# Kernel optimization log

Hardware: AMD Instinct MI355X
Metric: run time of the kernel (lower is better)

## Reference

```python
import jax, jax.numpy as jnp
import numpy as np

OUT, N_GROUPS, GROUP = 11008, 32, 128
IN = N_GROUPS * GROUP  # 4096
RANK = 128
B, S = 1, 64


def setup_inputs() -> dict:
    key = jax.random.key(0)
    ks = jax.random.split(key, 7)
    x = jax.random.normal(ks[0], (B, S, IN), dtype=jnp.float32)
    weight = jax.random.randint(ks[1], (OUT, N_GROUPS, GROUP), 0, 16, dtype=jnp.int32)
    scale = jax.random.uniform(ks[2], (OUT, N_GROUPS), dtype=jnp.float32) * 0.02 + 1e-3
    zero_point = jax.random.uniform(ks[3], (OUT, N_GROUPS), dtype=jnp.float32) * 15.0
    svd_up = jax.random.normal(ks[4], (OUT, RANK), dtype=jnp.float32) * 0.02
    svd_down = jax.random.normal(ks[5], (RANK, IN), dtype=jnp.float32) * 0.02
    bias = jax.random.normal(ks[6], (OUT,), dtype=jnp.float32) * 0.01
    return {"x": x, "weight": weight, "scale": scale, "zero_point": zero_point,
            "svd_up": svd_up, "svd_down": svd_down, "bias": bias}


def _dequantize(weight, scale, zero_point, svd_up, svd_down):
    # group-wise dequant: (W_q - zp) * scale, per (out, group) pair
    W = (weight.astype(jnp.float32) - zero_point[:, :, None]) * scale[:, :, None]
    W = W.reshape(weight.shape[0], -1)  # [OUT, IN]
    # low-rank SVD correction
    return W + svd_up @ svd_down


def reference(x, weight, scale, zero_point, svd_up, svd_down, bias):
    # int8 dynamic-quant path (token count 64 >= 16, int8_matmul=True)
    xt = x.reshape(-1, x.shape[-1])                       # [T, IN]
    W_f = _dequantize(weight, scale, zero_point, svd_up, svd_down).T  # [IN, OUT]
    scale_x = jnp.max(jnp.abs(xt), axis=1, keepdims=True) / 127.0     # [T, 1]
    x_q = jnp.clip(jnp.round(xt / scale_x), -128, 127).astype(jnp.int8)
    scale_w = jnp.max(jnp.abs(W_f), axis=0, keepdims=True) / 127.0    # [1, OUT]
    W_q8 = jnp.clip(jnp.round(W_f / scale_w), -128, 127).astype(jnp.int8)
    acc = jnp.matmul(x_q, W_q8, preferred_element_type=jnp.int32)     # [T, OUT] int32
    out = acc.astype(jnp.float32) * scale_x * scale_w
    return out[None] + bias  # [1, T, OUT], matching torch's unsqueeze(0) + bias
```

## Files before the change

### kernel.cpp

```cpp
#include <hip/hip_runtime.h>
#include <string.h>

#define OUT_DIM 11008
#define IN_DIM  4096
#define NTOK    64
#define RANK    128
#define NG      32
#define KSPLIT  8

typedef float        v4f  __attribute__((ext_vector_type(4)));
typedef int          v4i  __attribute__((ext_vector_type(4)));
typedef unsigned int v4u  __attribute__((ext_vector_type(4)));
typedef unsigned int v2u  __attribute__((ext_vector_type(2)));
typedef _Float16     v8h  __attribute__((ext_vector_type(8)));

__device__ inline unsigned int pack2h(float lo, float hi) {
  union { _Float16 h[2]; unsigned int u; } t;
  t.h[0] = (_Float16)lo; t.h[1] = (_Float16)hi;
  return t.u;
}

__global__ __launch_bounds__(256) void pack_d_kernel(const float* __restrict__ d,
                                                     unsigned int* __restrict__ dp) {
  int idx = (blockIdx.x * 256 + threadIdx.x) * 4;
  int r2 = idx >> 12, c = idx & 4095;
  v4f a = *(const v4f*)(d + (2 * r2) * IN_DIM + c);
  v4f b = *(const v4f*)(d + (2 * r2 + 1) * IN_DIM + c);
  v4u o;
#pragma unroll
  for (int e = 0; e < 4; e++) o[e] = pack2h(a[e], b[e]);
  *(v4u*)(dp + idx) = o;
}

__device__ inline void load_u(const float* __restrict__ svd_up, _Float16 (*U)[136],
                              int tid, int r0) {
#pragma unroll
  for (int i = 0; i < 16; i++) {
    int idx = i * 256 + tid;
    int r = idx >> 7, k = idx & 127;
    U[r][k] = (_Float16)svd_up[(r0 + r) * RANK + k];
  }
}

__device__ inline void stage_d(const unsigned int* __restrict__ dp, unsigned int (*Dl)[128],
                               int tid, int kt) {
  int c = (tid & 31) * 4;
#pragma unroll
  for (int i = 0; i < 8; i++) {
    int r2 = i * 8 + (tid >> 5);
    *(v4u*)&Dl[r2][c] = *(const v4u*)(dp + r2 * IN_DIM + kt * 128 + c);
  }
}

__device__ inline void svd_mfma(const _Float16 (*U)[136], const unsigned int (*Dl)[128],
                                int l, int w, v4f acc[2][2]) {
#pragma unroll
  for (int ks = 0; ks < 4; ks++) {
    v8h a0 = *(const v8h*)&U[(l & 15)][ks * 32 + (l >> 4) * 8];
    v8h a1 = *(const v8h*)&U[16 + (l & 15)][ks * 32 + (l >> 4) * 8];
#pragma unroll
    for (int fn = 0; fn < 2; fn++) {
      int col = w * 32 + fn * 16 + (l & 15);
      int rb = ks * 16 + (l >> 4) * 4;
      union { unsigned int u[4]; v8h h; } bu;
      bu.u[0] = Dl[rb][col];
      bu.u[1] = Dl[rb + 1][col];
      bu.u[2] = Dl[rb + 2][col];
      bu.u[3] = Dl[rb + 3][col];
      acc[0][fn] = __builtin_amdgcn_mfma_f32_16x16x32_f16(a0, bu.h, acc[0][fn], 0, 0, 0);
      acc[1][fn] = __builtin_amdgcn_mfma_f32_16x16x32_f16(a1, bu.h, acc[1][fn], 0, 0, 0);
    }
  }
}

__global__ __launch_bounds__(256) void cgemm_kernel(const float* __restrict__ svd_up,
    const unsigned int* __restrict__ dp, _Float16* __restrict__ Cb) {
  __shared__ _Float16 U[32][136];
  __shared__ unsigned int Dl[64][128];
  __shared__ _Float16 Clh[32][136];
  int tid = threadIdx.x;
  int r0 = blockIdx.x * 32;
  load_u(svd_up, U, tid, r0);
  int l = tid & 63, w = tid >> 6;
  int srow = tid >> 3, sc = (tid & 7) * 16;
  __syncthreads();
  for (int ct = 0; ct < 4; ct++) {
    int ktile = blockIdx.y * 4 + ct;
    stage_d(dp, Dl, tid, ktile);
    __syncthreads();
    v4f acc[2][2] = {};
    svd_mfma(U, Dl, l, w, acc);
#pragma unroll
    for (int fm = 0; fm < 2; fm++)
#pragma unroll
      for (int fn = 0; fn < 2; fn++)
#pragma unroll
        for (int j = 0; j < 4; j++)
          Clh[fm * 16 + (l >> 4) * 4 + j][w * 32 + fn * 16 + (l & 15)] = (_Float16)acc[fm][fn][j];
    __syncthreads();
    _Float16* dst = Cb + (r0 + srow) * IN_DIM + ktile * 128 + sc;
    *(v4u*)dst       = *(const v4u*)&Clh[srow][sc];
    *(v4u*)(dst + 8) = *(const v4u*)&Clh[srow][sc + 8];
  }
}

__global__ __launch_bounds__(256) void rowmax_kernel(const int* __restrict__ wq,
    const float* __restrict__ scale, const float* __restrict__ zp,
    const _Float16* __restrict__ Cb, unsigned int* __restrict__ wpk,
    float* __restrict__ swmax) {
  int tid = threadIdx.x;
  int lane = tid & 63, w = tid >> 6;
  int r = blockIdx.x * 4 + w;
  const int* wrow = wq + r * IN_DIM;
  const _Float16* crow = Cb + r * IN_DIM;
  unsigned int* prow = wpk + r * (IN_DIM / 8);
  const float* srow = scale + r * NG;
  const float* zrow = zp + r * NG;
  float m = 0.f;
#pragma unroll 4
  for (int j = 0; j < 8; j++) {
    int d = j * 64 + lane;
    int e0 = d * 8;
    v4i w0 = *(const v4i*)(wrow + e0);
    v4i w1 = *(const v4i*)(wrow + e0 + 4);
    union { v4u u; _Float16 h[8]; } cc;
    cc.u = *(const v4u*)(crow + e0);
    int g = e0 >> 7;
    float s = srow[g], z = zrow[g];
    unsigned int o = (unsigned)(w0[0] & 15)         | ((unsigned)(w0[1] & 15) << 4)
                   | ((unsigned)(w0[2] & 15) << 8)  | ((unsigned)(w0[3] & 15) << 12)
                   | ((unsigned)(w1[0] & 15) << 16) | ((unsigned)(w1[1] & 15) << 20)
                   | ((unsigned)(w1[2] & 15) << 24) | ((unsigned)(w1[3] & 15) << 28);
    prow[d] = o;
#pragma unroll
    for (int k = 0; k < 4; k++) {
      m = fmaxf(m, fabsf(((float)w0[k] - z) * s + (float)cc.h[k]));
      m = fmaxf(m, fabsf(((float)w1[k] - z) * s + (float)cc.h[k + 4]));
    }
  }
#pragma unroll
  for (int off = 1; off < 64; off <<= 1) m = fmaxf(m, __shfl_xor(m, off));
  if (lane == 0) swmax[r] = m;
}

__global__ __launch_bounds__(256) void quant_x_kernel(const float* __restrict__ x,
                                                      signed char* __restrict__ xq,
                                                      float* __restrict__ sx) {
  int t = blockIdx.x, tid = threadIdx.x;
  const float* row = x + t * IN_DIM;
  v4f v[4];
  float m = 0.f;
#pragma unroll
  for (int i = 0; i < 4; i++) {
    v[i] = *(const v4f*)(row + tid * 16 + i * 4);
#pragma unroll
    for (int e = 0; e < 4; e++) m = fmaxf(m, fabsf(v[i][e]));
  }
#pragma unroll
  for (int off = 1; off < 64; off <<= 1) m = fmaxf(m, __shfl_xor(m, off));
  __shared__ float wm[4];
  if ((tid & 63) == 0) wm[tid >> 6] = m;
  __syncthreads();
  m = fmaxf(fmaxf(wm[0], wm[1]), fmaxf(wm[2], wm[3]));
  float s = m / 127.0f;
  if (tid == 0) sx[t] = s;
  unsigned int packed[4];
#pragma unroll
  for (int i = 0; i < 4; i++) {
    int q[4];
#pragma unroll
    for (int e = 0; e < 4; e++) {
      float qf = rintf(v[i][e] / s);
      qf = fminf(127.f, fmaxf(-128.f, qf));
      q[e] = (int)qf;
    }
    packed[i] = (q[0] & 255) | ((q[1] & 255) << 8) | ((q[2] & 255) << 16) | ((q[3] & 255) << 24);
  }
  *(v4u*)(xq + t * IN_DIM + tid * 16) = *(v4u*)packed;
}

__global__ __launch_bounds__(256) void matmul_kernel(const unsigned int* __restrict__ wpk,
    const float* __restrict__ scale, const float* __restrict__ zp,
    const _Float16* __restrict__ Cb, const signed char* __restrict__ xq,
    const float* __restrict__ swmax, int* __restrict__ pacc) {
  __shared__ unsigned int W8[32][33];
  int tid = threadIdx.x;
  int r0 = blockIdx.x * 32;
  int kc = blockIdx.y;
  int l = tid & 63, w = tid >> 6;
  int myrow = tid >> 3, c0 = (tid & 7) * 16;
  float swr = swmax[r0 + myrow] / 127.0f;
  v4i oacc[2] = {};
  for (int kt = 0; kt < 4; kt++) {
    int kbase = kc * 512 + kt * 128;
    int g = kbase >> 7;
    float s = scale[(r0 + myrow) * NG + g];
    float z = zp[(r0 + myrow) * NG + g];
    v2u pk = *(const v2u*)(wpk + (r0 + myrow) * (IN_DIM / 8) + ((kbase + c0) >> 3));
    union { v4u u[2]; _Float16 h[16]; } cc;
    cc.u[0] = *(const v4u*)(Cb + (r0 + myrow) * IN_DIM + kbase + c0);
    cc.u[1] = *(const v4u*)(Cb + (r0 + myrow) * IN_DIM + kbase + c0 + 8);
    unsigned int wd[4];
#pragma unroll
    for (int i = 0; i < 4; i++) {
      int q[4];
#pragma unroll
      for (int e = 0; e < 4; e++) {
        int jj = i * 4 + e;
        int qn = (pk[jj >> 3] >> (4 * (jj & 7))) & 15;
        float W = ((float)qn - z) * s + (float)cc.h[jj];
        float qf = rintf(W / swr);
        qf = fminf(127.f, fmaxf(-128.f, qf));
        q[e] = (int)qf;
      }
      wd[i] = (q[0] & 255) | ((q[1] & 255) << 8) | ((q[2] & 255) << 16) | ((q[3] & 255) << 24);
    }
    __syncthreads();
#pragma unroll
    for (int i = 0; i < 4; i++) W8[myrow][(c0 >> 2) + i] = wd[i];
    __syncthreads();
#pragma unroll
    for (int ks = 0; ks < 2; ks++) {
      v4i a = *(const v4i*)(xq + (w * 16 + (l & 15)) * IN_DIM + kbase + ks * 64 + (l >> 4) * 16);
#pragma unroll
      for (int fr = 0; fr < 2; fr++) {
        int rr = fr * 16 + (l & 15);
        int kd = ks * 16 + (l >> 4) * 4;
        v4i b;
        b[0] = (int)W8[rr][kd];
        b[1] = (int)W8[rr][kd + 1];
        b[2] = (int)W8[rr][kd + 2];
        b[3] = (int)W8[rr][kd + 3];
        oacc[fr] = __builtin_amdgcn_mfma_i32_16x16x64_i8(a, b, oacc[fr], 0, 0, 0);
      }
    }
  }
  int* slab = pacc + kc * (NTOK * OUT_DIM);
#pragma unroll
  for (int fr = 0; fr < 2; fr++)
#pragma unroll
    for (int j = 0; j < 4; j++) {
      int token = w * 16 + (l >> 4) * 4 + j;
      int orow = r0 + fr * 16 + (l & 15);
      slab[token * OUT_DIM + orow] = oacc[fr][j];
    }
}

__global__ __launch_bounds__(256) void epilogue_kernel(const int* __restrict__ pacc,
    const float* __restrict__ sx, const float* __restrict__ swmax,
    const float* __restrict__ bias, float* __restrict__ out) {
  int o = blockIdx.x * 256 + threadIdx.x;
  int t = blockIdx.y;
  int acc = 0;
#pragma unroll
  for (int kc = 0; kc < KSPLIT; kc++)
    acc += pacc[kc * (NTOK * OUT_DIM) + t * OUT_DIM + o];
  float swv = swmax[o] / 127.0f;
  out[t * OUT_DIM + o] = (float)acc * sx[t] * swv + bias[o];
}

extern "C" void kernel_launch(void* const* d_in, const int* in_sizes, int n_in,
                              void* d_out, int out_size, void* d_ws, size_t ws_size,
                              hipStream_t stream) {
  (void)in_sizes; (void)n_in; (void)out_size; (void)ws_size;
  const float* x        = (const float*)d_in[0];
  const int*   wq       = (const int*)d_in[1];
  const float* scale    = (const float*)d_in[2];
  const float* zp       = (const float*)d_in[3];
  const float* svd_up   = (const float*)d_in[4];
  const float* svd_down = (const float*)d_in[5];
  const float* bias     = (const float*)d_in[6];
  float* out = (float*)d_out;

  char* ws = (char*)d_ws;
  unsigned int* dp    = (unsigned int*)(ws);
  signed char*  xq    = (signed char*)(ws + 1048576);
  float*        sx    = (float*)(ws + 1310720);
  float*        swmax = (float*)(ws + 1310976);
  unsigned int* wpk   = (unsigned int*)(ws + 1355008);
  _Float16*     Cb    = (_Float16*)(ws + 23899392);
  int*          pacc  = (int*)(ws + 114076928);

  pack_d_kernel<<<256, 256, 0, stream>>>(svd_down, dp);
  quant_x_kernel<<<NTOK, 256, 0, stream>>>(x, xq, sx);
  cgemm_kernel<<<dim3(OUT_DIM / 32, 8), 256, 0, stream>>>(svd_up, dp, Cb);
  rowmax_kernel<<<OUT_DIM / 4, 256, 0, stream>>>(wq, scale, zp, Cb, wpk, swmax);
  matmul_kernel<<<dim3(OUT_DIM / 32, KSPLIT), 256, 0, stream>>>(wpk, scale, zp, Cb, xq, swmax, pacc);
  epilogue_kernel<<<dim3(OUT_DIM / 256, NTOK), 256, 0, stream>>>(pacc, sx, swmax, bias, out);
}
```

Baseline: 353.3 us.

## Fuse SVD correction GEMM with dequant and partial row-max into one kernel

The SVD low-rank GEMM kernel now also reads the int32 weights, dequantizes them, adds the correction from shared memory, writes the full fp16 weight, and records a per-row partial max for each K chunk. A small kernel then reduces those partial maxes. The matmul kernel just loads the fp16 weight and no longer does nibble unpacking or dequant. This removes the separate rowmax pass that re-read the correction buffer and wrote packed nibbles. In exchange the fused kernel carries more register and memory traffic, and full fp16 weights are stored rounded after the correction is added.

```diff
diff --git a/kernel.cpp b/kernel.cpp
--- a/kernel.cpp
+++ b/kernel.cpp
@@ -7,6 +7,7 @@
 #define RANK    128
 #define NG      32
 #define KSPLIT  8
+#define KC      4
 
 typedef float        v4f  __attribute__((ext_vector_type(4)));
 typedef int          v4i  __attribute__((ext_vector_type(4)));
@@ -73,19 +74,23 @@
   }
 }
 
-__global__ __launch_bounds__(256) void cgemm_kernel(const float* __restrict__ svd_up,
-    const unsigned int* __restrict__ dp, _Float16* __restrict__ Cb) {
+__global__ __launch_bounds__(256, 3) void wsvd_kernel(const int* __restrict__ wq,
+    const float* __restrict__ scale, const float* __restrict__ zp,
+    const float* __restrict__ svd_up, const unsigned int* __restrict__ dp,
+    _Float16* __restrict__ Wf, float* __restrict__ pmax) {
   __shared__ _Float16 U[32][136];
   __shared__ unsigned int Dl[64][128];
   __shared__ _Float16 Clh[32][136];
   int tid = threadIdx.x;
   int r0 = blockIdx.x * 32;
+  int kc = blockIdx.y;
   load_u(svd_up, U, tid, r0);
   int l = tid & 63, w = tid >> 6;
-  int srow = tid >> 3, sc = (tid & 7) * 16;
+  int myrow = tid >> 3, c0 = (tid & 7) * 16;
+  float m = 0.f;
   __syncthreads();
-  for (int ct = 0; ct < 4; ct++) {
-    int ktile = blockIdx.y * 4 + ct;
+  for (int kt = 0; kt < 8; kt++) {
+    int ktile = kc * 8 + kt;
     stage_d(dp, Dl, tid, ktile);
     __syncthreads();
     v4f acc[2][2] = {};
@@ -98,49 +103,41 @@
         for (int j = 0; j < 4; j++)
           Clh[fm * 16 + (l >> 4) * 4 + j][w * 32 + fn * 16 + (l & 15)] = (_Float16)acc[fm][fn][j];
     __syncthreads();
-    _Float16* dst = Cb + (r0 + srow) * IN_DIM + ktile * 128 + sc;
-    *(v4u*)dst       = *(const v4u*)&Clh[srow][sc];
-    *(v4u*)(dst + 8) = *(const v4u*)&Clh[srow][sc + 8];
-  }
-}
-
-__global__ __launch_bounds__(256) void rowmax_kernel(const int* __restrict__ wq,
-    const float* __restrict__ scale, const float* __restrict__ zp,
-    const _Float16* __restrict__ Cb, unsigned int* __restrict__ wpk,
-    float* __restrict__ swmax) {
-  int tid = threadIdx.x;
-  int lane = tid & 63, w = tid >> 6;
-  int r = blockIdx.x * 4 + w;
-  const int* wrow = wq + r * IN_DIM;
-  const _Float16* crow = Cb + r * IN_DIM;
-  unsigned int* prow = wpk + r * (IN_DIM / 8);
-  const float* srow = scale + r * NG;
-  const float* zrow = zp + r * NG;
+    int e0 = ktile * 128 + c0;
+    float s = scale[(r0 + myrow) * NG + ktile];
+    float z = zp[(r0 + myrow) * NG + ktile];
+    v4i w0 = *(const v4i*)(wq + (r0 + myrow) * IN_DIM + e0);
+    v4i w1 = *(const v4i*)(wq + (r0 + myrow) * IN_DIM + e0 + 4);
+    v4i w2 = *(const v4i*)(wq + (r0 + myrow) * IN_DIM + e0 + 8);
+    v4i w3 = *(const v4i*)(wq + (r0 + myrow) * IN_DIM + e0 + 12);
+    union { v4u u[2]; _Float16 h[16]; } oo;
+#pragma unroll
+    for (int e = 0; e < 4; e++) {
+      float Wa = ((float)w0[e] - z) * s + (float)Clh[myrow][c0 + e];
+      float Wb = ((float)w1[e] - z) * s + (float)Clh[myrow][c0 + 4 + e];
+      float Wc = ((float)w2[e] - z) * s + (float)Clh[myrow][c0 + 8 + e];
+      float Wd = ((float)w3[e] - z) * s + (float)Clh[myrow][c0 + 12 + e];
+      m = fmaxf(m, fmaxf(fmaxf(fabsf(Wa), fabsf(Wb)), fmaxf(fabsf(Wc), fabsf(Wd))));
+      oo.h[e] = (_Float16)Wa; oo.h[4 + e] = (_Float16)Wb;
+      oo.h[8 + e] = (_Float16)Wc; oo.h[12 + e] = (_Float16)Wd;
+    }
+    _Float16* dst = Wf + (r0 + myrow) * IN_DIM + e0;
+    *(v4u*)dst = oo.u[0];
+    *(v4u*)(dst + 8) = oo.u[1];
+  }
+  m = fmaxf(m, __shfl_xor(m, 1));
+  m = fmaxf(m, __shfl_xor(m, 2));
+  m = fmaxf(m, __shfl_xor(m, 4));
+  if ((tid & 7) == 0) pmax[kc * OUT_DIM + r0 + myrow] = m;
+}
+
+__global__ __launch_bounds__(256) void maxfinish_kernel(const float* __restrict__ pmax,
+                                                        float* __restrict__ swmax) {
+  int r = blockIdx.x * 256 + threadIdx.x;
   float m = 0.f;
-#pragma unroll 4
-  for (int j = 0; j < 8; j++) {
-    int d = j * 64 + lane;
-    int e0 = d * 8;
-    v4i w0 = *(const v4i*)(wrow + e0);
-    v4i w1 = *(const v4i*)(wrow + e0 + 4);
-    union { v4u u; _Float16 h[8]; } cc;
-    cc.u = *(const v4u*)(crow + e0);
-    int g = e0 >> 7;
-    float s = srow[g], z = zrow[g];
-    unsigned int o = (unsigned)(w0[0] & 15)         | ((unsigned)(w0[1] & 15) << 4)
-                   | ((unsigned)(w0[2] & 15) << 8)  | ((unsigned)(w0[3] & 15) << 12)
-                   | ((unsigned)(w1[0] & 15) << 16) | ((unsigned)(w1[1] & 15) << 20)
-                   | ((unsigned)(w1[2] & 15) << 24) | ((unsigned)(w1[3] & 15) << 28);
-    prow[d] = o;
-#pragma unroll
-    for (int k = 0; k < 4; k++) {
-      m = fmaxf(m, fabsf(((float)w0[k] - z) * s + (float)cc.h[k]));
-      m = fmaxf(m, fabsf(((float)w1[k] - z) * s + (float)cc.h[k + 4]));
-    }
-  }
-#pragma unroll
-  for (int off = 1; off < 64; off <<= 1) m = fmaxf(m, __shfl_xor(m, off));
-  if (lane == 0) swmax[r] = m;
+#pragma unroll
+  for (int kc = 0; kc < KC; kc++) m = fmaxf(m, pmax[kc * OUT_DIM + r]);
+  swmax[r] = m;
 }
 
 __global__ __launch_bounds__(256) void quant_x_kernel(const float* __restrict__ x,
@@ -179,10 +176,9 @@
   *(v4u*)(xq + t * IN_DIM + tid * 16) = *(v4u*)packed;
 }
 
-__global__ __launch_bounds__(256) void matmul_kernel(const unsigned int* __restrict__ wpk,
-    const float* __restrict__ scale, const float* __restrict__ zp,
-    const _Float16* __restrict__ Cb, const signed char* __restrict__ xq,
-    const float* __restrict__ swmax, int* __restrict__ pacc) {
+__global__ __launch_bounds__(256) void matmul_kernel(const _Float16* __restrict__ Wf,
+    const signed char* __restrict__ xq, const float* __restrict__ swmax,
+    int* __restrict__ pacc) {
   __shared__ unsigned int W8[32][33];
   int tid = threadIdx.x;
   int r0 = blockIdx.x * 32;
@@ -193,22 +189,16 @@
   v4i oacc[2] = {};
   for (int kt = 0; kt < 4; kt++) {
     int kbase = kc * 512 + kt * 128;
-    int g = kbase >> 7;
-    float s = scale[(r0 + myrow) * NG + g];
-    float z = zp[(r0 + myrow) * NG + g];
-    v2u pk = *(const v2u*)(wpk + (r0 + myrow) * (IN_DIM / 8) + ((kbase + c0) >> 3));
     union { v4u u[2]; _Float16 h[16]; } cc;
-    cc.u[0] = *(const v4u*)(Cb + (r0 + myrow) * IN_DIM + kbase + c0);
-    cc.u[1] = *(const v4u*)(Cb + (r0 + myrow) * IN_DIM + kbase + c0 + 8);
+    cc.u[0] = *(const v4u*)(Wf + (r0 + myrow) * IN_DIM + kbase + c0);
+    cc.u[1] = *(const v4u*)(Wf + (r0 + myrow) * IN_DIM + kbase + c0 + 8);
     unsigned int wd[4];
 #pragma unroll
     for (int i = 0; i < 4; i++) {
       int q[4];
 #pragma unroll
       for (int e = 0; e < 4; e++) {
-        int jj = i * 4 + e;
-        int qn = (pk[jj >> 3] >> (4 * (jj & 7))) & 15;
-        float W = ((float)qn - z) * s + (float)cc.h[jj];
+        float W = (float)cc.h[i * 4 + e];
         float qf = rintf(W / swr);
         qf = fminf(127.f, fmaxf(-128.f, qf));
         q[e] = (int)qf;
@@ -277,14 +267,14 @@
   signed char*  xq    = (signed char*)(ws + 1048576);
   float*        sx    = (float*)(ws + 1310720);
   float*        swmax = (float*)(ws + 1310976);
-  unsigned int* wpk   = (unsigned int*)(ws + 1355008);
-  _Float16*     Cb    = (_Float16*)(ws + 23899392);
-  int*          pacc  = (int*)(ws + 114076928);
+  float*        pmax  = (float*)(ws + 1355008);
+  _Float16*     Wf    = (_Float16*)(ws + 1531136);
+  int*          pacc  = (int*)(ws + 91708672);
 
   pack_d_kernel<<<256, 256, 0, stream>>>(svd_down, dp);
   quant_x_kernel<<<NTOK, 256, 0, stream>>>(x, xq, sx);
-  cgemm_kernel<<<dim3(OUT_DIM / 32, 8), 256, 0, stream>>>(svd_up, dp, Cb);
-  rowmax_kernel<<<OUT_DIM / 4, 256, 0, stream>>>(wq, scale, zp, Cb, wpk, swmax);
-  matmul_kernel<<<dim3(OUT_DIM / 32, KSPLIT), 256, 0, stream>>>(wpk, scale, zp, Cb, xq, swmax, pacc);
+  wsvd_kernel<<<dim3(OUT_DIM / 32, KC), 256, 0, stream>>>(wq, scale, zp, svd_up, dp, Wf, pmax);
+  maxfinish_kernel<<<OUT_DIM / 256, 256, 0, stream>>>(pmax, swmax);
+  matmul_kernel<<<dim3(OUT_DIM / 32, KSPLIT), 256, 0, stream>>>(Wf, xq, swmax, pacc);
   epilogue_kernel<<<dim3(OUT_DIM / 256, NTOK), 256, 0, stream>>>(pacc, sx, swmax, bias, out);
 }
```

Measured after the change: 364.4 us. 3.1% more time.

## Quantize weights to int8 once in row pass; stream int8 directly in matmul

Applied to the files above, without the earlier changes.

The row-max kernel now keeps the dequantized weights in registers, computes the per-row scale, and writes the final int8 weight matrix directly. The matmul then loads int8 operands straight from global memory without re-dequantizing, re-reading the fp16 SVD correction, or staging through LDS. The split-K factor is halved, which shrinks the partial-sum slabs. The costs are a larger int8 intermediate write than the int4 pack and higher register pressure in the row kernel.

```diff
diff --git a/kernel.cpp b/kernel.cpp
--- a/kernel.cpp
+++ b/kernel.cpp
@@ -6,12 +6,11 @@
 #define NTOK    64
 #define RANK    128
 #define NG      32
-#define KSPLIT  8
+#define KSPLIT  4
 
 typedef float        v4f  __attribute__((ext_vector_type(4)));
 typedef int          v4i  __attribute__((ext_vector_type(4)));
 typedef unsigned int v4u  __attribute__((ext_vector_type(4)));
-typedef unsigned int v2u  __attribute__((ext_vector_type(2)));
 typedef _Float16     v8h  __attribute__((ext_vector_type(8)));
 
 __device__ inline unsigned int pack2h(float lo, float hi) {
@@ -104,43 +103,59 @@
   }
 }
 
-__global__ __launch_bounds__(256) void rowmax_kernel(const int* __restrict__ wq,
+__global__ __launch_bounds__(256) void wstream_kernel(const int* __restrict__ wq,
     const float* __restrict__ scale, const float* __restrict__ zp,
-    const _Float16* __restrict__ Cb, unsigned int* __restrict__ wpk,
+    const _Float16* __restrict__ Cb, signed char* __restrict__ W8,
     float* __restrict__ swmax) {
   int tid = threadIdx.x;
-  int lane = tid & 63, w = tid >> 6;
-  int r = blockIdx.x * 4 + w;
+  int lane = tid & 63;
+  int r = blockIdx.x * 4 + (tid >> 6);
   const int* wrow = wq + r * IN_DIM;
   const _Float16* crow = Cb + r * IN_DIM;
-  unsigned int* prow = wpk + r * (IN_DIM / 8);
-  const float* srow = scale + r * NG;
-  const float* zrow = zp + r * NG;
+  float W[4][16];
   float m = 0.f;
-#pragma unroll 4
-  for (int j = 0; j < 8; j++) {
-    int d = j * 64 + lane;
-    int e0 = d * 8;
-    v4i w0 = *(const v4i*)(wrow + e0);
-    v4i w1 = *(const v4i*)(wrow + e0 + 4);
-    union { v4u u; _Float16 h[8]; } cc;
-    cc.u = *(const v4u*)(crow + e0);
-    int g = e0 >> 7;
-    float s = srow[g], z = zrow[g];
-    unsigned int o = (unsigned)(w0[0] & 15)         | ((unsigned)(w0[1] & 15) << 4)
-                   | ((unsigned)(w0[2] & 15) << 8)  | ((unsigned)(w0[3] & 15) << 12)
-                   | ((unsigned)(w1[0] & 15) << 16) | ((unsigned)(w1[1] & 15) << 20)
-                   | ((unsigned)(w1[2] & 15) << 24) | ((unsigned)(w1[3] & 15) << 28);
-    prow[d] = o;
-#pragma unroll
-    for (int k = 0; k < 4; k++) {
-      m = fmaxf(m, fabsf(((float)w0[k] - z) * s + (float)cc.h[k]));
-      m = fmaxf(m, fabsf(((float)w1[k] - z) * s + (float)cc.h[k + 4]));
-    }
+#pragma unroll
+  for (int g = 0; g < 4; g++) {
+    int k0 = 1024 * g + 16 * lane;
+    v4i w0 = *(const v4i*)(wrow + k0);
+    v4i w1 = *(const v4i*)(wrow + k0 + 4);
+    v4i w2 = *(const v4i*)(wrow + k0 + 8);
+    v4i w3 = *(const v4i*)(wrow + k0 + 12);
+    union { v4u u[2]; _Float16 h[16]; } cc;
+    cc.u[0] = *(const v4u*)(crow + k0);
+    cc.u[1] = *(const v4u*)(crow + k0 + 8);
+    float s = scale[r * NG + 8 * g + (lane >> 3)];
+    float z = zp[r * NG + 8 * g + (lane >> 3)];
+#pragma unroll
+    for (int e = 0; e < 4; e++) {
+      W[g][e]      = ((float)w0[e] - z) * s + (float)cc.h[e];
+      W[g][4 + e]  = ((float)w1[e] - z) * s + (float)cc.h[4 + e];
+      W[g][8 + e]  = ((float)w2[e] - z) * s + (float)cc.h[8 + e];
+      W[g][12 + e] = ((float)w3[e] - z) * s + (float)cc.h[12 + e];
+    }
+#pragma unroll
+    for (int e = 0; e < 16; e++) m = fmaxf(m, fabsf(W[g][e]));
   }
 #pragma unroll
   for (int off = 1; off < 64; off <<= 1) m = fmaxf(m, __shfl_xor(m, off));
   if (lane == 0) swmax[r] = m;
+  float swr = m / 127.0f;
+#pragma unroll
+  for (int g = 0; g < 4; g++) {
+    int q[16];
+#pragma unroll
+    for (int e = 0; e < 16; e++) {
+      float qf = rintf(W[g][e] / swr);
+      qf = fminf(127.f, fmaxf(-128.f, qf));
+      q[e] = (int)qf;
+    }
+    v4u o;
+#pragma unroll
+    for (int i = 0; i < 4; i++)
+      o[i] = (q[4 * i] & 255) | ((q[4 * i + 1] & 255) << 8)
+           | ((q[4 * i + 2] & 255) << 16) | ((q[4 * i + 3] & 255) << 24);
+    *(v4u*)(W8 + r * IN_DIM + 1024 * g + 16 * lane) = o;
+  }
 }
 
 __global__ __launch_bounds__(256) void quant_x_kernel(const float* __restrict__ x,
@@ -179,61 +194,24 @@
   *(v4u*)(xq + t * IN_DIM + tid * 16) = *(v4u*)packed;
 }
 
-__global__ __launch_bounds__(256) void matmul_kernel(const unsigned int* __restrict__ wpk,
-    const float* __restrict__ scale, const float* __restrict__ zp,
-    const _Float16* __restrict__ Cb, const signed char* __restrict__ xq,
-    const float* __restrict__ swmax, int* __restrict__ pacc) {
-  __shared__ unsigned int W8[32][33];
+__global__ __launch_bounds__(256) void matmul_kernel(const signed char* __restrict__ W8,
+    const signed char* __restrict__ xq, int* __restrict__ pacc) {
   int tid = threadIdx.x;
   int r0 = blockIdx.x * 32;
   int kc = blockIdx.y;
   int l = tid & 63, w = tid >> 6;
-  int myrow = tid >> 3, c0 = (tid & 7) * 16;
-  float swr = swmax[r0 + myrow] / 127.0f;
+  const signed char* arow = xq + (w * 16 + (l & 15)) * IN_DIM + (l >> 4) * 16;
+  const signed char* brow0 = W8 + (r0 + (l & 15)) * IN_DIM + (l >> 4) * 16;
+  const signed char* brow1 = brow0 + 16 * IN_DIM;
   v4i oacc[2] = {};
-  for (int kt = 0; kt < 4; kt++) {
-    int kbase = kc * 512 + kt * 128;
-    int g = kbase >> 7;
-    float s = scale[(r0 + myrow) * NG + g];
-    float z = zp[(r0 + myrow) * NG + g];
-    v2u pk = *(const v2u*)(wpk + (r0 + myrow) * (IN_DIM / 8) + ((kbase + c0) >> 3));
-    union { v4u u[2]; _Float16 h[16]; } cc;
-    cc.u[0] = *(const v4u*)(Cb + (r0 + myrow) * IN_DIM + kbase + c0);
-    cc.u[1] = *(const v4u*)(Cb + (r0 + myrow) * IN_DIM + kbase + c0 + 8);
-    unsigned int wd[4];
-#pragma unroll
-    for (int i = 0; i < 4; i++) {
-      int q[4];
-#pragma unroll
-      for (int e = 0; e < 4; e++) {
-        int jj = i * 4 + e;
-        int qn = (pk[jj >> 3] >> (4 * (jj & 7))) & 15;
-        float W = ((float)qn - z) * s + (float)cc.h[jj];
-        float qf = rintf(W / swr);
-        qf = fminf(127.f, fmaxf(-128.f, qf));
-        q[e] = (int)qf;
-      }
-      wd[i] = (q[0] & 255) | ((q[1] & 255) << 8) | ((q[2] & 255) << 16) | ((q[3] & 255) << 24);
-    }
-    __syncthreads();
-#pragma unroll
-    for (int i = 0; i < 4; i++) W8[myrow][(c0 >> 2) + i] = wd[i];
-    __syncthreads();
-#pragma unroll
-    for (int ks = 0; ks < 2; ks++) {
-      v4i a = *(const v4i*)(xq + (w * 16 + (l & 15)) * IN_DIM + kbase + ks * 64 + (l >> 4) * 16);
-#pragma unroll
-      for (int fr = 0; fr < 2; fr++) {
-        int rr = fr * 16 + (l & 15);
-        int kd = ks * 16 + (l >> 4) * 4;
-        v4i b;
-        b[0] = (int)W8[rr][kd];
-        b[1] = (int)W8[rr][kd + 1];
-        b[2] = (int)W8[rr][kd + 2];
-        b[3] = (int)W8[rr][kd + 3];
-        oacc[fr] = __builtin_amdgcn_mfma_i32_16x16x64_i8(a, b, oacc[fr], 0, 0, 0);
-      }
-    }
+#pragma unroll 4
+  for (int kt = 0; kt < 16; kt++) {
+    int k0 = kc * 1024 + kt * 64;
+    v4i a  = *(const v4i*)(arow + k0);
+    v4i b0 = *(const v4i*)(brow0 + k0);
+    v4i b1 = *(const v4i*)(brow1 + k0);
+    oacc[0] = __builtin_amdgcn_mfma_i32_16x16x64_i8(a, b0, oacc[0], 0, 0, 0);
+    oacc[1] = __builtin_amdgcn_mfma_i32_16x16x64_i8(a, b1, oacc[1], 0, 0, 0);
   }
   int* slab = pacc + kc * (NTOK * OUT_DIM);
 #pragma unroll
@@ -256,7 +234,7 @@
   for (int kc = 0; kc < KSPLIT; kc++)
     acc += pacc[kc * (NTOK * OUT_DIM) + t * OUT_DIM + o];
   float swv = swmax[o] / 127.0f;
-  out[t * OUT_DIM + o] = (float)acc * sx[t] * swv + bias[o];
+  out[t * OUT_DIM + o] = ((float)acc * sx[t]) * swv + bias[o];
 }
 
 extern "C" void kernel_launch(void* const* d_in, const int* in_sizes, int n_in,
@@ -277,14 +255,14 @@
   signed char*  xq    = (signed char*)(ws + 1048576);
   float*        sx    = (float*)(ws + 1310720);
   float*        swmax = (float*)(ws + 1310976);
-  unsigned int* wpk   = (unsigned int*)(ws + 1355008);
-  _Float16*     Cb    = (_Float16*)(ws + 23899392);
-  int*          pacc  = (int*)(ws + 114076928);
+  _Float16*     Cb    = (_Float16*)(ws + 1355008);
+  signed char*  W8    = (signed char*)(ws + 91532544);
+  int*          pacc  = (int*)(ws + 136621312);
 
   pack_d_kernel<<<256, 256, 0, stream>>>(svd_down, dp);
   quant_x_kernel<<<NTOK, 256, 0, stream>>>(x, xq, sx);
   cgemm_kernel<<<dim3(OUT_DIM / 32, 8), 256, 0, stream>>>(svd_up, dp, Cb);
-  rowmax_kernel<<<OUT_DIM / 4, 256, 0, stream>>>(wq, scale, zp, Cb, wpk, swmax);
-  matmul_kernel<<<dim3(OUT_DIM / 32, KSPLIT), 256, 0, stream>>>(wpk, scale, zp, Cb, xq, swmax, pacc);
+  wstream_kernel<<<OUT_DIM / 4, 256, 0, stream>>>(wq, scale, zp, Cb, W8, swmax);
+  matmul_kernel<<<dim3(OUT_DIM / 32, KSPLIT), 256, 0, stream>>>(W8, xq, pacc);
   epilogue_kernel<<<dim3(OUT_DIM / 256, NTOK), 256, 0, stream>>>(pacc, sx, swmax, bias, out);
 }
```

Result: no change. 358.5 us (+1.5%).
